# Optimization experiments

Measured on AMD Instinct MI355X. Metric: run time of the kernel, lower is better.

The kernel has to match this reference:

```python
import jax, jax.numpy as jnp
import numpy as np

B = 32          # batch (decoding sequences)
HID = 4096      # hidden_size
NH = 32         # num query heads
NKV = 8         # num kv heads
HS = 128        # head_size
BS = 16         # paged-cache block size
MAXS = 2048     # max context length
MAXB = MAXS // BS            # blocks per sequence
NBLOCKS = B * MAXB           # total cache blocks
ROPE_BASE = 10000.0


def rope(x, pos):
    # NeoX rotate-half RoPE (offset = head_size//2, rotary_ndims = head_size).
    # x: [T, n_head, HS], pos: [T] int
    half = x.shape[-1] // 2
    inv_freq = 1.0 / (ROPE_BASE ** (jnp.arange(half, dtype=jnp.float32) * 2.0 / (2 * half)))
    freqs = pos[:, None].astype(jnp.float32) * inv_freq[None, :]   # [T, half]
    cos = jnp.cos(freqs)[:, None, :]
    sin = jnp.sin(freqs)[:, None, :]
    x1, x2 = x[..., :half], x[..., half:]
    return jnp.concatenate([x1 * cos - x2 * sin, x2 * cos + x1 * sin], axis=-1)


def setup_inputs() -> dict:
    key = jax.random.key(0)
    ks = jax.random.split(key, 8)
    hidden_states = jax.random.normal(ks[0], (B, 1, HID), jnp.float32)
    wq = jax.random.normal(ks[1], (NH * HS, HID), jnp.float32) * 0.02
    wk = jax.random.normal(ks[2], (NKV * HS, HID), jnp.float32) * 0.02
    wv = jax.random.normal(ks[3], (NKV * HS, HID), jnp.float32) * 0.02
    wo = jax.random.normal(ks[4], (NH * HS, NH * HS), jnp.float32) * 0.02
    k_cache = jax.random.normal(ks[5], (NBLOCKS, BS, NKV, HS), jnp.float32)
    v_cache = jax.random.normal(ks[6], (NBLOCKS, BS, NKV, HS), jnp.float32)
    # each sequence owns a disjoint set of MAXB blocks
    block_tables = jnp.arange(NBLOCKS, dtype=jnp.int32).reshape(B, MAXB)
    input_lengths = jax.random.randint(ks[7], (B,), 1, MAXS + 1, jnp.int32)
    position_ids = (input_lengths - 1).astype(jnp.int64)  # decode: write at last position
    last = input_lengths - 1
    slots = (block_tables[jnp.arange(B), last // BS] * BS + last % BS).astype(jnp.int32)
    return {
        "hidden_states": hidden_states, "wq": wq, "wk": wk, "wv": wv, "wo": wo,
        "k_cache": k_cache, "v_cache": v_cache, "position_ids": position_ids,
        "block_tables": block_tables, "slots": slots,
        "input_lengths": input_lengths, "max_s": MAXS,
    }


def reference(hidden_states, wq, wk, wv, wo, k_cache, v_cache,
              position_ids, block_tables, slots, input_lengths, max_s):
    bsz, q_len, hid = hidden_states.shape
    x = hidden_states.reshape(bsz * q_len, hid)
    q = (x @ wq.T).reshape(-1, NH, HS)
    k = (x @ wk.T).reshape(-1, NKV, HS)
    v = (x @ wv.T).reshape(-1, NKV, HS)
    q = rope(q, position_ids)
    k = rope(k, position_ids)
    # reshape_and_cache: scatter rope'd k and v into paged cache at slot indices
    kc = k_cache.reshape(-1, NKV, HS).at[slots].set(k)   # [NBLOCKS*BS, NKV, HS]
    vc = v_cache.reshape(-1, NKV, HS).at[slots].set(v)
    # single-query paged attention: gather per-sequence K/V via block_tables
    flat_idx = (block_tables[:, :, None] * BS
                + jnp.arange(BS, dtype=block_tables.dtype)[None, None, :]).reshape(bsz, -1)  # [B, max_s]
    keys = kc[flat_idx]    # [B, S, NKV, HS]
    vals = vc[flat_idx]    # [B, S, NKV, HS]
    groups = NH // NKV
    qg = q.reshape(bsz, NKV, groups, HS)
    scale = HS ** -0.5
    scores = jnp.einsum('bhgd,bshd->bhgs', qg, keys) * scale       # [B, NKV, G, S]
    valid = jnp.arange(max_s)[None, :] < input_lengths[:, None]    # [B, S]
    scores = jnp.where(valid[:, None, None, :], scores, -jnp.inf)
    p = jax.nn.softmax(scores, axis=-1)
    attn = jnp.einsum('bhgs,bshd->bhgd', p, vals).reshape(bsz, NH * HS)
    return (attn @ wo.T).reshape(bsz, q_len, hid)
```

## Files before the change

kernel.cpp:

```cpp
#include <hip/hip_runtime.h>
#include <math.h>


__device__ __forceinline__ void gemm_body(
    const float* __restrict__ x, const float* __restrict__ w,
    float* __restrict__ dst, int dstride, int kbase, int kcnt)
{
    __shared__ float xs[32][36];
    __shared__ float wsm[32][257];
    int t = threadIdx.x;
    float acc[4][8];
#pragma unroll
    for (int i = 0; i < 4; ++i)
#pragma unroll
        for (int j = 0; j < 8; ++j) acc[i][j] = 0.f;

    int nsub = t & 31, bsub = t >> 5;

    for (int kt = 0; kt < kcnt; kt += 32) {
        int k0 = kbase + kt;
        {
            int b = t >> 3, k4 = (t & 7) << 2;
            float4 xv = *(const float4*)(x + (size_t)b * 4096 + k0 + k4);
            *(float4*)&xs[b][k4] = xv;
        }
        {
            int k4 = (t & 7) << 2;
            int nl0 = t >> 3;
#pragma unroll
            for (int i = 0; i < 8; ++i) {
                int nl = nl0 + (i << 5);
                float4 wv = *(const float4*)(w + (size_t)nl * 4096 + k0 + k4);
                wsm[k4 + 0][nl] = wv.x;
                wsm[k4 + 1][nl] = wv.y;
                wsm[k4 + 2][nl] = wv.z;
                wsm[k4 + 3][nl] = wv.w;
            }
        }
        __syncthreads();
#pragma unroll
        for (int k = 0; k < 32; ++k) {
            float xv[4], wv[8];
#pragma unroll
            for (int j = 0; j < 4; ++j) xv[j] = xs[bsub * 4 + j][k];
#pragma unroll
            for (int j = 0; j < 8; ++j) wv[j] = wsm[k][nsub + (j << 5)];
#pragma unroll
            for (int jb = 0; jb < 4; ++jb)
#pragma unroll
                for (int jn = 0; jn < 8; ++jn)
                    acc[jb][jn] = fmaf(xv[jb], wv[jn], acc[jb][jn]);
        }
        __syncthreads();
    }
#pragma unroll
    for (int jb = 0; jb < 4; ++jb) {
        int b = bsub * 4 + jb;
#pragma unroll
        for (int jn = 0; jn < 8; ++jn)
            atomicAdd(dst + (size_t)b * dstride + nsub + (jn << 5), acc[jb][jn]);
    }
}

__global__ __launch_bounds__(256) void qkv_gemm(
    const float* __restrict__ x, const float* __restrict__ wq,
    const float* __restrict__ wk, const float* __restrict__ wv,
    float* __restrict__ qb, float* __restrict__ knb, float* __restrict__ vnb)
{
    int split = blockIdx.x & 15;
    int tile  = blockIdx.x >> 4;
    const float* w; float* dst; int dstride;
    if (tile < 16)      { w = wq + (size_t)tile * 256 * 4096;        dst = qb  + tile * 256;        dstride = 4096; }
    else if (tile < 20) { w = wk + (size_t)(tile - 16) * 256 * 4096; dst = knb + (tile - 16) * 256; dstride = 1024; }
    else                { w = wv + (size_t)(tile - 20) * 256 * 4096; dst = vnb + (tile - 20) * 256; dstride = 1024; }
    gemm_body(x, w, dst, dstride, split * 256, 256);
}

__global__ __launch_bounds__(256) void wo_gemm(
    const float* __restrict__ attn, const float* __restrict__ wo,
    float* __restrict__ out)
{
    int split = blockIdx.x & 15;
    int tile  = blockIdx.x >> 4;
    gemm_body(attn, wo + (size_t)tile * 256 * 4096, out + tile * 256, 4096, split * 256, 256);
}

__global__ void rope_kernel(float* __restrict__ qb, float* __restrict__ knb,
                            const int* __restrict__ lens)
{
    int bid = blockIdx.x;
    int b = bid / 40, r = bid % 40;
    float* row = (r < 32) ? (qb + (size_t)b * 4096 + r * 128)
                          : (knb + (size_t)b * 1024 + (r - 32) * 128);
    int d = threadIdx.x;
    float pos = (float)(lens[b] - 1);
    float inv = exp2f(-(float)d * 0.207620505930460f);
    float fr = pos * inv;
    float s, c;
    sincosf(fr, &s, &c);
    float x1 = row[d], x2 = row[d + 64];
    row[d]      = x1 * c - x2 * s;
    row[d + 64] = x2 * c + x1 * s;
}

#define MUL4(V, S) { V.x *= S; V.y *= S; V.z *= S; V.w *= S; }
#define FMA4(O, P, V) { O.x = fmaf(P, V.x, O.x); O.y = fmaf(P, V.y, O.y); \
                        O.z = fmaf(P, V.z, O.z); O.w = fmaf(P, V.w, O.w); }
#define DOT8(S, QA, QB, K0, K1) { \
    S = fmaf(QA.x, K0.x, S); S = fmaf(QA.y, K0.y, S); \
    S = fmaf(QA.z, K0.z, S); S = fmaf(QA.w, K0.w, S); \
    S = fmaf(QB.x, K1.x, S); S = fmaf(QB.y, K1.y, S); \
    S = fmaf(QB.z, K1.z, S); S = fmaf(QB.w, K1.w, S); }
#define RED16(X) { X += __shfl_xor(X, 1, 64); X += __shfl_xor(X, 2, 64); \
                   X += __shfl_xor(X, 4, 64); X += __shfl_xor(X, 8, 64); }
#define REDG_SUM(X) { X += __shfl_xor(X, 16, 64); X += __shfl_xor(X, 32, 64); }
#define REDG_MAX(X) { X = fmaxf(X, __shfl_xor(X, 16, 64)); \
                      X = fmaxf(X, __shfl_xor(X, 32, 64)); }
#define REDG_SUM4(V) { REDG_SUM(V.x) REDG_SUM(V.y) REDG_SUM(V.z) REDG_SUM(V.w) }

#define ALOADR(S, r_) { \
    int sl = ss[((r_) << 2) + g]; \
    const float* kp; const float* vp; \
    if (sl < 0) { kp = knew; vp = vnew; } \
    else { kp = kc + (size_t)sl * 1024 + hoff; vp = vc + (size_t)sl * 1024 + hoff; } \
    S##k0 = *(const float4*)(kp + isl); S##k1 = *(const float4*)(kp + isl + 4); \
    S##v0 = *(const float4*)(vp + isl); S##v1 = *(const float4*)(vp + isl + 4); }

#define ACOMP(S, r_) { \
    float s0 = 0.f, s1 = 0.f, s2 = 0.f, s3 = 0.f; \
    DOT8(s0, q0a, q0b, S##k0, S##k1) \
    DOT8(s1, q1a, q1b, S##k0, S##k1) \
    DOT8(s2, q2a, q2b, S##k0, S##k1) \
    DOT8(s3, q3a, q3b, S##k0, S##k1) \
    RED16(s0) RED16(s1) RED16(s2) RED16(s3) \
    if (((r_) << 2) + g >= pend) { s0 = s1 = s2 = s3 = -INFINITY; } \
    float r0 = s0, r1 = s1, r2 = s2, r3 = s3; \
    REDG_MAX(r0) REDG_MAX(r1) REDG_MAX(r2) REDG_MAX(r3) \
    if (r0 > m0 || r1 > m1 || r2 > m2 || r3 > m3) { \
        float n0 = fmaxf(m0, r0), n1 = fmaxf(m1, r1); \
        float n2 = fmaxf(m2, r2), n3 = fmaxf(m3, r3); \
        float c0 = __expf(m0 - n0), c1 = __expf(m1 - n1); \
        float c2 = __expf(m2 - n2), c3 = __expf(m3 - n3); \
        l0 *= c0; l1 *= c1; l2 *= c2; l3 *= c3; \
        MUL4(o0a, c0) MUL4(o0b, c0) MUL4(o1a, c1) MUL4(o1b, c1) \
        MUL4(o2a, c2) MUL4(o2b, c2) MUL4(o3a, c3) MUL4(o3b, c3) \
        m0 = n0; m1 = n1; m2 = n2; m3 = n3; \
    } \
    float pe0 = __expf(s0 - m0), pe1 = __expf(s1 - m1); \
    float pe2 = __expf(s2 - m2), pe3 = __expf(s3 - m3); \
    float t0 = pe0, t1 = pe1, t2 = pe2, t3 = pe3; \
    REDG_SUM(t0) REDG_SUM(t1) REDG_SUM(t2) REDG_SUM(t3) \
    l0 += t0; l1 += t1; l2 += t2; l3 += t3; \
    FMA4(o0a, pe0, S##v0) FMA4(o0b, pe0, S##v1) \
    FMA4(o1a, pe1, S##v0) FMA4(o1b, pe1, S##v1) \
    FMA4(o2a, pe2, S##v0) FMA4(o2b, pe2, S##v1) \
    FMA4(o3a, pe3, S##v0) FMA4(o3b, pe3, S##v1) }

__global__ __launch_bounds__(64, 1) void attn_kernel(
    const float* __restrict__ kc, const float* __restrict__ vc,
    const float* __restrict__ qb, const float* __restrict__ knb,
    const float* __restrict__ vnb,
    const int* __restrict__ btab, const int* __restrict__ lens,
    float* __restrict__ part)
{
    int bid = blockIdx.x;
    int c = bid & 7, h = (bid >> 3) & 7, b = bid >> 6;
    int len = lens[b];
    int p0 = c << 8;
    if (p0 >= len) return;
    int pend = min(len - p0, 256);
    int nr = (pend + 3) >> 2;
    int last = len - 1;

    __shared__ int ss[256];

    int lane = threadIdx.x;
    int g = lane >> 4;
    int isl = (lane & 15) << 3;
    int hoff = h * 128;

    {
        int idx = lane << 2;
        int p = p0 + idx;
        int bt = btab[b * 128 + (p >> 4)];
        int base = bt * 16 + (p & 15);
        ss[idx]     = (p     == last) ? -1 : base;
        ss[idx + 1] = (p + 1 == last) ? -1 : base + 1;
        ss[idx + 2] = (p + 2 == last) ? -1 : base + 2;
        ss[idx + 3] = (p + 3 == last) ? -1 : base + 3;
    }

    const float* knew = knb + ((size_t)b * 8 + h) * 128;
    const float* vnew = vnb + ((size_t)b * 8 + h) * 128;

    const float scale = 0.08838834764831845f;
    const float* qrow = qb + (size_t)b * 4096 + (size_t)h * 512;
    float4 q0a = *(const float4*)(qrow + isl),       q0b = *(const float4*)(qrow + isl + 4);
    float4 q1a = *(const float4*)(qrow + 128 + isl), q1b = *(const float4*)(qrow + 128 + isl + 4);
    float4 q2a = *(const float4*)(qrow + 256 + isl), q2b = *(const float4*)(qrow + 256 + isl + 4);
    float4 q3a = *(const float4*)(qrow + 384 + isl), q3b = *(const float4*)(qrow + 384 + isl + 4);
    MUL4(q0a, scale) MUL4(q0b, scale) MUL4(q1a, scale) MUL4(q1b, scale)
    MUL4(q2a, scale) MUL4(q2b, scale) MUL4(q3a, scale) MUL4(q3b, scale)

    float m0 = -INFINITY, m1 = -INFINITY, m2 = -INFINITY, m3 = -INFINITY;
    float l0 = 0.f, l1 = 0.f, l2 = 0.f, l3 = 0.f;
    float4 o0a = {0,0,0,0}, o0b = {0,0,0,0}, o1a = {0,0,0,0}, o1b = {0,0,0,0};
    float4 o2a = {0,0,0,0}, o2b = {0,0,0,0}, o3a = {0,0,0,0}, o3b = {0,0,0,0};

    float4 ak0, ak1, av0, av1, bk0, bk1, bv0, bv1;
    ALOADR(a, 0)
    for (int r = 0; r < nr; r += 2) {
        if (r + 1 < nr) ALOADR(b, r + 1)
        ACOMP(a, r)
        if (r + 1 >= nr) break;
        if (r + 2 < nr) ALOADR(a, r + 2)
        ACOMP(b, r + 1)
    }

    REDG_SUM4(o0a) REDG_SUM4(o0b) REDG_SUM4(o1a) REDG_SUM4(o1b)
    REDG_SUM4(o2a) REDG_SUM4(o2b) REDG_SUM4(o3a) REDG_SUM4(o3b)

    float* pgb = part + (size_t)(((b * 8 + h) * 8 + c) * 4) * 132;
    if (lane < 16) {
        *(float4*)(pgb +       isl) = o0a; *(float4*)(pgb +       isl + 4) = o0b;
        *(float4*)(pgb + 132 + isl) = o1a; *(float4*)(pgb + 132 + isl + 4) = o1b;
        *(float4*)(pgb + 264 + isl) = o2a; *(float4*)(pgb + 264 + isl + 4) = o2b;
        *(float4*)(pgb + 396 + isl) = o3a; *(float4*)(pgb + 396 + isl + 4) = o3b;
    }
    if (lane == 0) {
        pgb[128] = m0; pgb[129] = l0;
        pgb[260] = m1; pgb[261] = l1;
        pgb[392] = m2; pgb[393] = l2;
        pgb[524] = m3; pgb[525] = l3;
    }
}

__global__ __launch_bounds__(256) void combine_kernel(
    const float* __restrict__ part, const int* __restrict__ lens,
    float* __restrict__ attn)
{
    int b = blockIdx.x >> 3, h = blockIdx.x & 7;
    int t = threadIdx.x;
    int g = t >> 6, lane = t & 63;
    int len = lens[b];
    int nch = (len + 255) >> 8;
    const float* base = part + (size_t)(b * 8 + h) * 4224 + (size_t)g * 132;
    float M = -INFINITY;
    for (int cc = 0; cc < nch; ++cc)
        M = fmaxf(M, base[(size_t)cc * 528 + 128]);
    float denom = 0.f, a0 = 0.f, a1 = 0.f;
    int d0 = lane << 1;
    for (int cc = 0; cc < nch; ++cc) {
        const float* pg = base + (size_t)cc * 528;
        float w = __expf(pg[128] - M);
        denom += w * pg[129];
        a0 += w * pg[d0];
        a1 += w * pg[d0 + 1];
    }
    float inv = 1.f / denom;
    float* dst = attn + (size_t)b * 4096 + (size_t)(h * 4 + g) * 128 + d0;
    dst[0] = a0 * inv;
    dst[1] = a1 * inv;
}

extern "C" void kernel_launch(void* const* d_in, const int* in_sizes, int n_in,
                              void* d_out, int out_size, void* d_ws, size_t ws_size,
                              hipStream_t stream)
{
    const float* x   = (const float*)d_in[0];
    const float* wq  = (const float*)d_in[1];
    const float* wk  = (const float*)d_in[2];
    const float* wv  = (const float*)d_in[3];
    const float* wo  = (const float*)d_in[4];
    const float* kc  = (const float*)d_in[5];
    const float* vc  = (const float*)d_in[6];
    const int* btab  = (const int*)d_in[8];
    const int* lens  = (const int*)d_in[10];

    float* qb   = (float*)d_ws;
    float* knb  = qb  + 32 * 4096;
    float* vnb  = knb + 32 * 1024;
    float* attn = vnb + 32 * 1024;
    float* part = attn + 32 * 4096;
    float* outp = (float*)d_out;

    hipMemsetAsync(d_ws, 0, (size_t)(32 * 4096 + 2 * 32 * 1024) * sizeof(float), stream);
    hipMemsetAsync(d_out, 0, (size_t)32 * 4096 * sizeof(float), stream);

    qkv_gemm<<<24 * 16, 256, 0, stream>>>(x, wq, wk, wv, qb, knb, vnb);
    rope_kernel<<<32 * 40, 64, 0, stream>>>(qb, knb, lens);
    attn_kernel<<<2048, 64, 0, stream>>>(kc, vc, qb, knb, vnb, btab, lens, part);
    combine_kernel<<<256, 256, 0, stream>>>(part, lens, attn);
    wo_gemm<<<16 * 16, 256, 0, stream>>>(attn, wo, outp);
}
```

Before: 178.8 us.

## Split attention into 128-token chunks, per-group online softmax, triple-buffer K/V loads

The attention kernel now splits each sequence into 16 chunks of 128 tokens instead of 8 of 256, doubling the grid so more workgroups are in flight on short-context and long-context rows alike. Each 16-lane group now keeps its own running max and sum, so the per-row cross-group max and sum shuffles are dropped and replaced by a single merge after the loop. K/V loads are triple-buffered to keep more memory requests outstanding. The cost is more partial results for the combine kernel to merge and more registers held per thread.

New measurement: 178.1 us. No clear change (-0.4%).

```diff
diff --git a/kernel.cpp b/kernel.cpp
--- a/kernel.cpp
+++ b/kernel.cpp
@@ -126,6 +126,16 @@
     S##k0 = *(const float4*)(kp + isl); S##k1 = *(const float4*)(kp + isl + 4); \
     S##v0 = *(const float4*)(vp + isl); S##v1 = *(const float4*)(vp + isl + 4); }
 
+#define OUPD(s_, m_, l_, Oa_, Ob_, V0_, V1_, vld_) { \
+    if (s_ > m_) { \
+        float c_ = __expf(m_ - s_); \
+        l_ *= c_; MUL4(Oa_, c_) MUL4(Ob_, c_) \
+        m_ = s_; \
+    } \
+    float pe_ = vld_ ? __expf(s_ - m_) : 0.f; \
+    l_ += pe_; \
+    FMA4(Oa_, pe_, V0_) FMA4(Ob_, pe_, V1_) }
+
 #define ACOMP(S, r_) { \
     float s0 = 0.f, s1 = 0.f, s2 = 0.f, s3 = 0.f; \
     DOT8(s0, q0a, q0b, S##k0, S##k1) \
@@ -133,28 +143,12 @@
     DOT8(s2, q2a, q2b, S##k0, S##k1) \
     DOT8(s3, q3a, q3b, S##k0, S##k1) \
     RED16(s0) RED16(s1) RED16(s2) RED16(s3) \
-    if (((r_) << 2) + g >= pend) { s0 = s1 = s2 = s3 = -INFINITY; } \
-    float r0 = s0, r1 = s1, r2 = s2, r3 = s3; \
-    REDG_MAX(r0) REDG_MAX(r1) REDG_MAX(r2) REDG_MAX(r3) \
-    if (r0 > m0 || r1 > m1 || r2 > m2 || r3 > m3) { \
-        float n0 = fmaxf(m0, r0), n1 = fmaxf(m1, r1); \
-        float n2 = fmaxf(m2, r2), n3 = fmaxf(m3, r3); \
-        float c0 = __expf(m0 - n0), c1 = __expf(m1 - n1); \
-        float c2 = __expf(m2 - n2), c3 = __expf(m3 - n3); \
-        l0 *= c0; l1 *= c1; l2 *= c2; l3 *= c3; \
-        MUL4(o0a, c0) MUL4(o0b, c0) MUL4(o1a, c1) MUL4(o1b, c1) \
-        MUL4(o2a, c2) MUL4(o2b, c2) MUL4(o3a, c3) MUL4(o3b, c3) \
-        m0 = n0; m1 = n1; m2 = n2; m3 = n3; \
-    } \
-    float pe0 = __expf(s0 - m0), pe1 = __expf(s1 - m1); \
-    float pe2 = __expf(s2 - m2), pe3 = __expf(s3 - m3); \
-    float t0 = pe0, t1 = pe1, t2 = pe2, t3 = pe3; \
-    REDG_SUM(t0) REDG_SUM(t1) REDG_SUM(t2) REDG_SUM(t3) \
-    l0 += t0; l1 += t1; l2 += t2; l3 += t3; \
-    FMA4(o0a, pe0, S##v0) FMA4(o0b, pe0, S##v1) \
-    FMA4(o1a, pe1, S##v0) FMA4(o1b, pe1, S##v1) \
-    FMA4(o2a, pe2, S##v0) FMA4(o2b, pe2, S##v1) \
-    FMA4(o3a, pe3, S##v0) FMA4(o3b, pe3, S##v1) }
+    int vld = (((r_) << 2) + g) < pend; \
+    if (!vld) { s0 = s1 = s2 = s3 = -INFINITY; } \
+    OUPD(s0, m0, l0, o0a, o0b, S##v0, S##v1, vld) \
+    OUPD(s1, m1, l1, o1a, o1b, S##v0, S##v1, vld) \
+    OUPD(s2, m2, l2, o2a, o2b, S##v0, S##v1, vld) \
+    OUPD(s3, m3, l3, o3a, o3b, S##v0, S##v1, vld) }
 
 __global__ __launch_bounds__(64, 1) void attn_kernel(
     const float* __restrict__ kc, const float* __restrict__ vc,
@@ -164,15 +158,15 @@
     float* __restrict__ part)
 {
     int bid = blockIdx.x;
-    int c = bid & 7, h = (bid >> 3) & 7, b = bid >> 6;
+    int c = bid & 15, h = (bid >> 4) & 7, b = bid >> 7;
     int len = lens[b];
-    int p0 = c << 8;
+    int p0 = c << 7;
     if (p0 >= len) return;
-    int pend = min(len - p0, 256);
+    int pend = min(len - p0, 128);
     int nr = (pend + 3) >> 2;
     int last = len - 1;
 
-    __shared__ int ss[256];
+    __shared__ int ss[128];
 
     int lane = threadIdx.x;
     int g = lane >> 4;
@@ -180,14 +174,12 @@
     int hoff = h * 128;
 
     {
-        int idx = lane << 2;
+        int idx = lane << 1;
         int p = p0 + idx;
         int bt = btab[b * 128 + (p >> 4)];
         int base = bt * 16 + (p & 15);
         ss[idx]     = (p     == last) ? -1 : base;
         ss[idx + 1] = (p + 1 == last) ? -1 : base + 1;
-        ss[idx + 2] = (p + 2 == last) ? -1 : base + 2;
-        ss[idx + 3] = (p + 3 == last) ? -1 : base + 3;
     }
 
     const float* knew = knb + ((size_t)b * 8 + h) * 128;
@@ -207,20 +199,35 @@
     float4 o0a = {0,0,0,0}, o0b = {0,0,0,0}, o1a = {0,0,0,0}, o1b = {0,0,0,0};
     float4 o2a = {0,0,0,0}, o2b = {0,0,0,0}, o3a = {0,0,0,0}, o3b = {0,0,0,0};
 
-    float4 ak0, ak1, av0, av1, bk0, bk1, bv0, bv1;
+    float4 ak0, ak1, av0, av1;
+    float4 bk0, bk1, bv0, bv1;
+    float4 ck0, ck1, cv0, cv1;
     ALOADR(a, 0)
-    for (int r = 0; r < nr; r += 2) {
-        if (r + 1 < nr) ALOADR(b, r + 1)
+    if (1 < nr) ALOADR(b, 1)
+    if (2 < nr) ALOADR(c, 2)
+    for (int r = 0; r < nr; r += 3) {
         ACOMP(a, r)
+        if (r + 3 < nr) ALOADR(a, r + 3)
         if (r + 1 >= nr) break;
-        if (r + 2 < nr) ALOADR(a, r + 2)
         ACOMP(b, r + 1)
-    }
-
+        if (r + 4 < nr) ALOADR(b, r + 4)
+        if (r + 2 >= nr) break;
+        ACOMP(c, r + 2)
+        if (r + 5 < nr) ALOADR(c, r + 5)
+    }
+
+    float M0 = m0, M1 = m1, M2 = m2, M3 = m3;
+    REDG_MAX(M0) REDG_MAX(M1) REDG_MAX(M2) REDG_MAX(M3)
+    float w0 = __expf(m0 - M0), w1 = __expf(m1 - M1);
+    float w2 = __expf(m2 - M2), w3 = __expf(m3 - M3);
+    float L0 = w0 * l0, L1 = w1 * l1, L2 = w2 * l2, L3 = w3 * l3;
+    REDG_SUM(L0) REDG_SUM(L1) REDG_SUM(L2) REDG_SUM(L3)
+    MUL4(o0a, w0) MUL4(o0b, w0) MUL4(o1a, w1) MUL4(o1b, w1)
+    MUL4(o2a, w2) MUL4(o2b, w2) MUL4(o3a, w3) MUL4(o3b, w3)
     REDG_SUM4(o0a) REDG_SUM4(o0b) REDG_SUM4(o1a) REDG_SUM4(o1b)
     REDG_SUM4(o2a) REDG_SUM4(o2b) REDG_SUM4(o3a) REDG_SUM4(o3b)
 
-    float* pgb = part + (size_t)(((b * 8 + h) * 8 + c) * 4) * 132;
+    float* pgb = part + (size_t)(((b * 8 + h) * 16 + c) * 4) * 132;
     if (lane < 16) {
         *(float4*)(pgb +       isl) = o0a; *(float4*)(pgb +       isl + 4) = o0b;
         *(float4*)(pgb + 132 + isl) = o1a; *(float4*)(pgb + 132 + isl + 4) = o1b;
@@ -228,10 +235,10 @@
         *(float4*)(pgb + 396 + isl) = o3a; *(float4*)(pgb + 396 + isl + 4) = o3b;
     }
     if (lane == 0) {
-        pgb[128] = m0; pgb[129] = l0;
-        pgb[260] = m1; pgb[261] = l1;
-        pgb[392] = m2; pgb[393] = l2;
-        pgb[524] = m3; pgb[525] = l3;
+        pgb[128] = M0; pgb[129] = L0;
+        pgb[260] = M1; pgb[261] = L1;
+        pgb[392] = M2; pgb[393] = L2;
+        pgb[524] = M3; pgb[525] = L3;
     }
 }
 
@@ -243,8 +250,8 @@
     int t = threadIdx.x;
     int g = t >> 6, lane = t & 63;
     int len = lens[b];
-    int nch = (len + 255) >> 8;
-    const float* base = part + (size_t)(b * 8 + h) * 4224 + (size_t)g * 132;
+    int nch = (len + 127) >> 7;
+    const float* base = part + (size_t)(b * 8 + h) * 8448 + (size_t)g * 132;
     float M = -INFINITY;
     for (int cc = 0; cc < nch; ++cc)
         M = fmaxf(M, base[(size_t)cc * 528 + 128]);
@@ -289,7 +296,7 @@
 
     qkv_gemm<<<24 * 16, 256, 0, stream>>>(x, wq, wk, wv, qb, knb, vnb);
     rope_kernel<<<32 * 40, 64, 0, stream>>>(qb, knb, lens);
-    attn_kernel<<<2048, 64, 0, stream>>>(kc, vc, qb, knb, vnb, btab, lens, part);
+    attn_kernel<<<4096, 64, 0, stream>>>(kc, vc, qb, knb, vnb, btab, lens, part);
     combine_kernel<<<256, 256, 0, stream>>>(part, lens, attn);
     wo_gemm<<<16 * 16, 256, 0, stream>>>(attn, wo, outp);
 }
```
